# Performance work log

Measured on AMD Instinct MI355X. Metric: run time of the kernel, lower is better.

The kernel has to match this reference:

```python
import jax, jax.numpy as jnp
import numpy as np

N, C, A = 4096, 1000, 64


def setup_inputs() -> dict:
    key = jax.random.key(0)
    k1, k2, k3, k4, k5 = jax.random.split(key, 5)
    weight_m = jax.random.normal(k1, (C, A), dtype=jnp.float32)
    y = jax.random.normal(k2, (N, C), dtype=jnp.float32)
    features = jax.random.normal(k3, (N, A), dtype=jnp.float32)
    target_x = jax.random.randint(k4, (N,), 0, C)
    ratio = jnp.float32(0.5)
    final_conv = jax.random.normal(k5, (N, A, A), dtype=jnp.float32) * 0.1
    return {
        "weight_m": weight_m,
        "y": y,
        "features": features,
        "target_x": target_x,
        "ratio": ratio,
        "final_conv": final_conv,
        "class_num": C,
    }


def reference(weight_m, y, features, target_x, ratio, final_conv, class_num):
    # weight_m: (C, A); y: (N, C); features: (N, A) (only supplies N, A)
    # target_x: (N,) int labels; final_conv: (N, A, A); ratio: scalar
    Wk = weight_m[target_x]                       # (N, A)  gather of label row
    d = weight_m[None, :, :] - Wk[:, None, :]     # (N, C, A) = NxW_ij - NxW_kj

    # sigma1 = ||w_j||^2 - ||w_{y_n}||^2
    w2 = jnp.sum(weight_m * weight_m, axis=-1)    # (C,)
    sigma1 = w2[None, :] - w2[target_x][:, None]  # (N, C)

    # sigma2 = ratio * diag(d @ CV @ d^T), computed directly (no NxCxC matrix)
    t = jnp.einsum('nca,nab->ncb', d, final_conv)  # (N, C, A)
    sigma2 = ratio * jnp.sum(t * d, axis=-1)       # (N, C)

    logits = y + 0.5 * sigma2 + sigma1             # (N, C)

    # mean cross-entropy (nn.CrossEntropyLoss default)
    logp = jax.nn.log_softmax(logits, axis=-1)
    nll = -jnp.take_along_axis(logp, target_x[:, None], axis=1)[:, 0]
    loss = jnp.mean(nll)
    return loss, y
```

## Files before the change

### kernel.cpp

```cpp
#include <hip/hip_runtime.h>
#include <hip/hip_bf16.h>
#include <stdint.h>
#include <stddef.h>

#define N_    4096
#define C_    1000
#define CP    1024
#define A_    64
#define KPACK 2080
#define KCROSS (KPACK + 64)
#define KTOT  2304
#define KQ    576
#define MS    68

typedef __bf16 bf16_2 __attribute__((ext_vector_type(2)));
typedef __bf16 bf16_8 __attribute__((ext_vector_type(8)));
typedef float  f32_4  __attribute__((ext_vector_type(4)));

__device__ __forceinline__ void gl2lds16(const void* g, void* l) {
  __builtin_amdgcn_global_load_lds(
      (const __attribute__((address_space(1))) void*)g,
      (__attribute__((address_space(3))) void*)l, 16, 0, 0);
}

__device__ __forceinline__ void unpack_pair(int k, int& a, int& b) {
  a = (int)(0.5f * (129.0f - sqrtf((float)(16641 - 8 * k))));
  if (a < 0) a = 0;
  while ((a + 1) * (129 - (a + 1)) / 2 <= k) ++a;
  while (a * (129 - a) / 2 > k) --a;
  b = k - a * (129 - a) / 2 + a;
}

__global__ __launch_bounds__(256) void prep_all(
    const float* __restrict__ W, const int* __restrict__ tgt,
    const float* __restrict__ CV, __bf16* __restrict__ Bo,
    float* __restrict__ w2, __bf16* __restrict__ Aq, float* __restrict__ qn) {
  __shared__ float Ms[64 * MS];
  __shared__ float up[4 * 64];
  __shared__ float wk[64];
  __shared__ float us[64];
  int t = threadIdx.x;

  if (blockIdx.x < 1024) {
    int c = blockIdx.x;
    float* ws = Ms;
    if (t < 64) {
      float w = (c < C_) ? W[c * 64 + t] : 0.f;
      ws[t] = w;
      float s = w * w;
      for (int o = 32; o; o >>= 1) s += __shfl_down(s, o);
      if (t == 0 && c < C_) w2[c] = s;
    }
    __syncthreads();
    __bf16* row = Bo + (size_t)c * KTOT;
    for (int p = t; p < KPACK / 2; p += 256) {
      int k = 2 * p;
      int a0, b0, a1, b1;
      unpack_pair(k, a0, b0);
      if (b0 == 63) { a1 = a0 + 1; b1 = a1; } else { a1 = a0; b1 = b0 + 1; }
      bf16_2 v;
      v[0] = (__bf16)(ws[a0] * ws[b0]);
      v[1] = (__bf16)(ws[a1] * ws[b1]);
      *(bf16_2*)(row + k) = v;
    }
    if (t < 64) row[KPACK + t] = (__bf16)ws[t];
    for (int z2 = t; z2 < KTOT - KCROSS; z2 += 256) row[KCROSS + z2] = (__bf16)0.f;
  } else {
    int n = blockIdx.x - 1024;
    int lbl = tgt[n];
    if (t < 64) wk[t] = W[lbl * 64 + t];
    const float4* M4 = (const float4*)(CV + (size_t)n * 4096);
    for (int j = 0; j < 4; ++j) {
      int i4 = t + j * 256;
      int r = i4 >> 4, c4 = (i4 & 15) << 2;
      *(float4*)&Ms[r * MS + c4] = M4[i4];
    }
    __syncthreads();
    {
      int a = t & 63, seg = t >> 6;
      float acc = 0.f;
      for (int b = seg * 16; b < seg * 16 + 16; ++b)
        acc += (Ms[a * MS + b] + Ms[b * MS + a]) * wk[b];
      up[seg * 64 + a] = acc;
    }
    __syncthreads();
    if (t < 64) {
      float u = up[t] + up[64 + t] + up[128 + t] + up[192 + t];
      us[t] = u;
      float p = wk[t] * u;
      for (int o = 32; o; o >>= 1) p += __shfl_down(p, o);
      if (t == 0) qn[n] = 0.5f * p;
    }
    __syncthreads();
    __bf16* row = Aq + (size_t)n * KTOT;
    for (int p = t; p < KPACK / 2; p += 256) {
      int k = 2 * p;
      int a0, b0, a1, b1;
      unpack_pair(k, a0, b0);
      if (b0 == 63) { a1 = a0 + 1; b1 = a1; } else { a1 = a0; b1 = b0 + 1; }
      bf16_2 v;
      v[0] = (__bf16)((a0 == b0) ? Ms[a0 * MS + a0]
                                 : (Ms[a0 * MS + b0] + Ms[b0 * MS + a0]));
      v[1] = (__bf16)((a1 == b1) ? Ms[a1 * MS + a1]
                                 : (Ms[a1 * MS + b1] + Ms[b1 * MS + a1]));
      *(bf16_2*)(row + k) = v;
    }
    if (t < 64) row[KPACK + t] = (__bf16)(-us[t]);
    for (int z2 = t; z2 < KTOT - KCROSS; z2 += 256) row[KCROSS + z2] = (__bf16)0.f;
  }
}

#define BM 128
#define BN 128
#define BK 64
__global__ __launch_bounds__(256) void gemm_s(const __bf16* __restrict__ Aq,
                                              const __bf16* __restrict__ Bo,
                                              __bf16* __restrict__ Sbase) {
  __shared__ __bf16 As[BM * BK];
  __shared__ __bf16 Bs[BN * BK];
  int t = threadIdx.x;
  int lane = t & 63;
  int w = t >> 6;
  int wr = w & 1;
  int wc = w >> 1;
  int rowBase = blockIdx.y * BM;
  int colBase = blockIdx.x * BN;
  int kb = blockIdx.z * KQ;
  __bf16* S = Sbase + (size_t)blockIdx.z * ((size_t)N_ * CP);

  f32_4 acc[4][4];
  for (int mi = 0; mi < 4; ++mi)
    for (int ni = 0; ni < 4; ++ni)
      acc[mi][ni] = (f32_4){0.f, 0.f, 0.f, 0.f};

  int m0 = lane & 15;
  int qsw = m0 & 7;

  for (int k0 = kb; k0 < kb + KQ; k0 += BK) {
    __syncthreads();
    for (int r = 0; r < 4; ++r) {
      int ch = r * 256 + t;
      int row_p = ch >> 3, qp = ch & 7;
      int q_log = qp ^ (row_p & 7);
      const __bf16* g = Aq + (size_t)(rowBase + row_p) * KTOT + k0 + (q_log << 3);
      gl2lds16(g, As + ch * 8);
    }
    for (int r = 0; r < 4; ++r) {
      int ch = r * 256 + t;
      int row_p = ch >> 3, qp = ch & 7;
      int q_log = qp ^ (row_p & 7);
      const __bf16* g = Bo + (size_t)(colBase + row_p) * KTOT + k0 + (q_log << 3);
      gl2lds16(g, Bs + ch * 8);
    }
    __syncthreads();
    for (int kk = 0; kk < BK; kk += 32) {
      int qbase = (kk >> 3) + (lane >> 4);
      int qphys = qbase ^ qsw;
      bf16_8 af[4], bf[4];
      for (int mi = 0; mi < 4; ++mi)
        af[mi] = *(const bf16_8*)&As[(wr * 64 + mi * 16 + m0) * BK + (qphys << 3)];
      for (int ni = 0; ni < 4; ++ni)
        bf[ni] = *(const bf16_8*)&Bs[(wc * 64 + ni * 16 + m0) * BK + (qphys << 3)];
      for (int mi = 0; mi < 4; ++mi)
        for (int ni = 0; ni < 4; ++ni)
          acc[mi][ni] = __builtin_amdgcn_mfma_f32_16x16x32_bf16(af[mi], bf[ni], acc[mi][ni], 0, 0, 0);
    }
  }

  int ccol = lane & 15;
  int rrow = (lane >> 4) * 4;
  for (int mi = 0; mi < 4; ++mi)
    for (int ni = 0; ni < 4; ++ni) {
      int r0 = rowBase + wr * 64 + mi * 16 + rrow;
      int c0 = colBase + wc * 64 + ni * 16 + ccol;
      for (int j = 0; j < 4; ++j)
        S[(size_t)(r0 + j) * CP + c0] = (__bf16)acc[mi][ni][j];
    }
}

__global__ __launch_bounds__(256) void epilogue(
    const __bf16* __restrict__ Sb, const float* __restrict__ y,
    const float* __restrict__ w2, const float* __restrict__ qn,
    const int* __restrict__ tgt, const float* __restrict__ ratio_p,
    float* __restrict__ nll) {
  int t = threadIdx.x, lane = t & 63, w = t >> 6;
  int n = blockIdx.x * 4 + w;
  float hr = 0.5f * (*ratio_p);
  int lbl = tgt[n];
  float q = qn[n];
  float w2k = w2[lbl];
  const bf16_8* S0 = (const bf16_8*)(Sb + (size_t)n * CP);
  const bf16_8* S1 = (const bf16_8*)(Sb + 1ull * N_ * CP + (size_t)n * CP);
  const bf16_8* S2 = (const bf16_8*)(Sb + 2ull * N_ * CP + (size_t)n * CP);
  const bf16_8* S3 = (const bf16_8*)(Sb + 3ull * N_ * CP + (size_t)n * CP);
  const float* yr = y + (size_t)n * C_;
  float l[16];
  float mx = -1e30f;
  for (int i = 0; i < 2; ++i) {
    int idx = i * 64 + lane;
    bf16_8 a0 = S0[idx], a1 = S1[idx], a2 = S2[idx], a3 = S3[idx];
    int c0 = idx * 8;
    for (int j = 0; j < 8; ++j) {
      int c = c0 + j;
      float v = -1e30f;
      if (c < C_) {
        float s = (float)a0[j] + (float)a1[j] + (float)a2[j] + (float)a3[j];
        v = yr[c] + (w2[c] - w2k) + hr * (s + q);
      }
      l[i * 8 + j] = v;
      mx = fmaxf(mx, v);
    }
  }
  for (int o = 32; o; o >>= 1) mx = fmaxf(mx, __shfl_xor(mx, o));
  float se = 0.f, lt = 0.f;
  for (int i = 0; i < 2; ++i) {
    int c0 = (i * 64 + lane) * 8;
    for (int j = 0; j < 8; ++j) {
      float v = l[i * 8 + j];
      se += expf(v - mx);
      lt += (c0 + j == lbl) ? v : 0.f;
    }
  }
  for (int o = 32; o; o >>= 1) {
    se += __shfl_xor(se, o);
    lt += __shfl_xor(lt, o);
  }
  if (lane == 0) nll[n] = (mx + logf(se)) - lt;
}

__global__ void reduce_loss(const float* __restrict__ nll, float* __restrict__ out) {
  int t = threadIdx.x;
  float s = 0.f;
  for (int i = t; i < N_; i += 256) s += nll[i];
  for (int o = 32; o; o >>= 1) s += __shfl_down(s, o);
  __shared__ float r[4];
  if ((t & 63) == 0) r[t >> 6] = s;
  __syncthreads();
  if (t == 0) out[0] = (r[0] + r[1] + r[2] + r[3]) * (1.0f / (float)N_);
}

extern "C" void kernel_launch(void* const* d_in, const int* in_sizes, int n_in,
                              void* d_out, int out_size, void* d_ws, size_t ws_size,
                              hipStream_t stream) {
  const float* W     = (const float*)d_in[0];
  const float* y     = (const float*)d_in[1];
  const int*   tgt   = (const int*)d_in[3];
  const float* ratio = (const float*)d_in[4];
  const float* CV    = (const float*)d_in[5];

  char* ws = (char*)d_ws;
  size_t off = 0;
  __bf16* Aq = (__bf16*)(ws + off); off += (size_t)N_ * KTOT * sizeof(__bf16);
  __bf16* Bo = (__bf16*)(ws + off); off += (size_t)CP * KTOT * sizeof(__bf16);
  __bf16* S  = (__bf16*)(ws + off); off += 4ull * N_ * CP * sizeof(__bf16);
  float* w2  = (float*)(ws + off);  off += 4096;
  float* qn  = (float*)(ws + off);  off += (size_t)N_ * sizeof(float);
  float* nll = (float*)(ws + off);  off += (size_t)N_ * sizeof(float);

  float* out = (float*)d_out;
  hipMemcpyAsync(out + 1, y, (size_t)N_ * C_ * sizeof(float),
                 hipMemcpyDeviceToDevice, stream);

  prep_all<<<1024 + N_, 256, 0, stream>>>(W, tgt, CV, Bo, w2, Aq, qn);
  gemm_s<<<dim3(CP / BN, N_ / BM, 4), 256, 0, stream>>>(Aq, Bo, S);
  epilogue<<<N_ / 4, 256, 0, stream>>>(S, y, w2, qn, tgt, ratio, nll);
  reduce_loss<<<1, 256, 0, stream>>>(nll, out);
}
```

Measured before the change: 188.8 us.

## Trim K padding, halve split-K, fuse y copy into epilogue

Shrinks the packed K dimension from 2304 to 2176 so less zero padding is loaded and multiplied, and cuts split-K from 4 to 2 partitions, halving the bf16 partial-sum buffer that is written and re-read. The separate device-to-device memcpy of y into the output is removed; the epilogue now writes y while it already reads it. The GEMM grid is reordered so consecutive blocks walk along N. The trade-off is fewer GEMM blocks and therefore less parallelism.

```diff
diff --git a/kernel.cpp b/kernel.cpp
--- a/kernel.cpp
+++ b/kernel.cpp
@@ -9,8 +9,8 @@
 #define A_    64
 #define KPACK 2080
 #define KCROSS (KPACK + 64)
-#define KTOT  2304
-#define KQ    576
+#define KTOT  2176
+#define KHALF 1088
 #define MS    68
 
 typedef __bf16 bf16_2 __attribute__((ext_vector_type(2)));
@@ -64,7 +64,7 @@
       *(bf16_2*)(row + k) = v;
     }
     if (t < 64) row[KPACK + t] = (__bf16)ws[t];
-    for (int z2 = t; z2 < KTOT - KCROSS; z2 += 256) row[KCROSS + z2] = (__bf16)0.f;
+    if (t >= 64 && t < 96) row[KCROSS + (t - 64)] = (__bf16)0.f;
   } else {
     int n = blockIdx.x - 1024;
     int lbl = tgt[n];
@@ -106,7 +106,7 @@
       *(bf16_2*)(row + k) = v;
     }
     if (t < 64) row[KPACK + t] = (__bf16)(-us[t]);
-    for (int z2 = t; z2 < KTOT - KCROSS; z2 += 256) row[KCROSS + z2] = (__bf16)0.f;
+    if (t >= 64 && t < 96) row[KCROSS + (t - 64)] = (__bf16)0.f;
   }
 }
 
@@ -123,9 +123,9 @@
   int w = t >> 6;
   int wr = w & 1;
   int wc = w >> 1;
-  int rowBase = blockIdx.y * BM;
-  int colBase = blockIdx.x * BN;
-  int kb = blockIdx.z * KQ;
+  int rowBase = blockIdx.x * BM;
+  int colBase = blockIdx.y * BN;
+  int kb = blockIdx.z * KHALF;
   __bf16* S = Sbase + (size_t)blockIdx.z * ((size_t)N_ * CP);
 
   f32_4 acc[4][4];
@@ -136,7 +136,7 @@
   int m0 = lane & 15;
   int qsw = m0 & 7;
 
-  for (int k0 = kb; k0 < kb + KQ; k0 += BK) {
+  for (int k0 = kb; k0 < kb + KHALF; k0 += BK) {
     __syncthreads();
     for (int r = 0; r < 4; ++r) {
       int ch = r * 256 + t;
@@ -182,7 +182,7 @@
     const __bf16* __restrict__ Sb, const float* __restrict__ y,
     const float* __restrict__ w2, const float* __restrict__ qn,
     const int* __restrict__ tgt, const float* __restrict__ ratio_p,
-    float* __restrict__ nll) {
+    float* __restrict__ nll, float* __restrict__ outy) {
   int t = threadIdx.x, lane = t & 63, w = t >> 6;
   int n = blockIdx.x * 4 + w;
   float hr = 0.5f * (*ratio_p);
@@ -191,26 +191,26 @@
   float w2k = w2[lbl];
   const bf16_8* S0 = (const bf16_8*)(Sb + (size_t)n * CP);
   const bf16_8* S1 = (const bf16_8*)(Sb + 1ull * N_ * CP + (size_t)n * CP);
-  const bf16_8* S2 = (const bf16_8*)(Sb + 2ull * N_ * CP + (size_t)n * CP);
-  const bf16_8* S3 = (const bf16_8*)(Sb + 3ull * N_ * CP + (size_t)n * CP);
   const float* yr = y + (size_t)n * C_;
+  float* oy = outy + (size_t)n * C_;
   float l[16];
   float mx = -1e30f;
   for (int i = 0; i < 2; ++i) {
     int idx = i * 64 + lane;
-    bf16_8 a0 = S0[idx], a1 = S1[idx], a2 = S2[idx], a3 = S3[idx];
+    bf16_8 a0 = S0[idx], a1 = S1[idx];
     int c0 = idx * 8;
     for (int j = 0; j < 8; ++j) {
       int c = c0 + j;
       float v = -1e30f;
       if (c < C_) {
-        float s = (float)a0[j] + (float)a1[j] + (float)a2[j] + (float)a3[j];
+        float s = (float)a0[j] + (float)a1[j];
         v = yr[c] + (w2[c] - w2k) + hr * (s + q);
       }
       l[i * 8 + j] = v;
       mx = fmaxf(mx, v);
     }
   }
+  for (int c = lane; c < C_; c += 64) oy[c] = yr[c];
   for (int o = 32; o; o >>= 1) mx = fmaxf(mx, __shfl_xor(mx, o));
   float se = 0.f, lt = 0.f;
   for (int i = 0; i < 2; ++i) {
@@ -252,17 +252,15 @@
   size_t off = 0;
   __bf16* Aq = (__bf16*)(ws + off); off += (size_t)N_ * KTOT * sizeof(__bf16);
   __bf16* Bo = (__bf16*)(ws + off); off += (size_t)CP * KTOT * sizeof(__bf16);
-  __bf16* S  = (__bf16*)(ws + off); off += 4ull * N_ * CP * sizeof(__bf16);
+  __bf16* S  = (__bf16*)(ws + off); off += 2ull * N_ * CP * sizeof(__bf16);
   float* w2  = (float*)(ws + off);  off += 4096;
   float* qn  = (float*)(ws + off);  off += (size_t)N_ * sizeof(float);
   float* nll = (float*)(ws + off);  off += (size_t)N_ * sizeof(float);
 
   float* out = (float*)d_out;
-  hipMemcpyAsync(out + 1, y, (size_t)N_ * C_ * sizeof(float),
-                 hipMemcpyDeviceToDevice, stream);
 
   prep_all<<<1024 + N_, 256, 0, stream>>>(W, tgt, CV, Bo, w2, Aq, qn);
-  gemm_s<<<dim3(CP / BN, N_ / BM, 4), 256, 0, stream>>>(Aq, Bo, S);
-  epilogue<<<N_ / 4, 256, 0, stream>>>(S, y, w2, qn, tgt, ratio, nll);
+  gemm_s<<<dim3(N_ / BM, CP / BN, 2), 256, 0, stream>>>(Aq, Bo, S);
+  epilogue<<<N_ / 4, 256, 0, stream>>>(S, y, w2, qn, tgt, ratio, nll, out + 1);
   reduce_loss<<<1, 256, 0, stream>>>(nll, out);
 }
```

After: 172.9 us. 1.09x faster.
